# Optimization experiments

Hardware: AMD Instinct MI355X
Metric: run time of the kernel (lower is better)

Reference implementation:

```python
import jax, jax.numpy as jnp
import numpy as np

N, D, S, E, EL, ITERS = 250_000, 128, 6, 500_000, 50_000, 4


def setup_inputs() -> dict:
    key = jax.random.key(0)
    ks = jax.random.split(key, 16)
    s = 1.0 / np.sqrt(D)  # keep activations O(1)
    return {
        'feat':   jax.random.normal(ks[0], (N, D), jnp.float32),
        'pre_u':  jax.random.randint(ks[1], (S, E), 0, N, jnp.int32),
        'pre_v':  jax.random.randint(ks[2], (S, E), 0, N, jnp.int32),
        'suc_u':  jax.random.randint(ks[3], (S, E), 0, N, jnp.int32),
        'suc_v':  jax.random.randint(ks[4], (S, E), 0, N, jnp.int32),
        'left_u': jax.random.randint(ks[5], (EL,), 0, N, jnp.int32),
        'left_v': jax.random.randint(ks[6], (EL,), 0, N, jnp.int32),
        'right_u': jax.random.randint(ks[7], (EL,), 0, N, jnp.int32),
        'right_v': jax.random.randint(ks[8], (EL,), 0, N, jnp.int32),
        'W_ctr':   jax.random.normal(ks[9],  (ITERS, D, D), jnp.float32) * s,
        'W_pre':   jax.random.normal(ks[10], (ITERS, S, D, D), jnp.float32) * s,
        'W_suc':   jax.random.normal(ks[11], (ITERS, S, D, D), jnp.float32) * s,
        'W_left':  jax.random.normal(ks[12], (ITERS, D, D), jnp.float32) * s,
        'W_right': jax.random.normal(ks[13], (ITERS, D, D), jnp.float32) * s,
        'gn1_w': jnp.ones((ITERS, D), jnp.float32),
        'gn1_b': jnp.zeros((ITERS, D), jnp.float32),
        'W_ctr2':  jax.random.normal(ks[14], (ITERS, D, D), jnp.float32) * s,
        'gn2_w': jnp.ones((ITERS, D), jnp.float32),
        'gn2_b': jnp.zeros((ITERS, D), jnp.float32),
    }


def _gn(x, w, b, eps=1e-5):
    # torch GroupNorm(1, D) on a [N, D] input: per-row normalization over channels
    mu = jnp.mean(x, -1, keepdims=True)
    var = jnp.mean((x - mu) ** 2, -1, keepdims=True)
    return (x - mu) * jax.lax.rsqrt(var + eps) * w + b


def reference(feat, pre_u, pre_v, suc_u, suc_v, left_u, left_v, right_u, right_v,
              W_ctr, W_pre, W_suc, W_left, W_right, gn1_w, gn1_b,
              W_ctr2, gn2_w, gn2_b):
    res = feat
    for i in range(ITERS):  # 4 fusion iterations, structurally distinct weights
        temp = feat @ W_ctr[i].T  # nn.Linear(bias=False): x @ W.T
        for k in range(S):  # 6 dilation scales, pre and suc edges
            temp = temp.at[pre_u[k]].add(feat[pre_v[k]] @ W_pre[i, k].T)
            temp = temp.at[suc_u[k]].add(feat[suc_v[k]] @ W_suc[i, k].T)
        temp = temp.at[left_u].add(feat[left_v] @ W_left[i].T)
        temp = temp.at[right_u].add(feat[right_v] @ W_right[i].T)
        h = jax.nn.relu(_gn(temp, gn1_w[i], gn1_b[i]))           # fuse['norm'] + relu
        h = _gn(h @ W_ctr2[i].T, gn2_w[i], gn2_b[i])             # fuse['ctr2']: Linear+GN, no act
        feat = jax.nn.relu(h + res)                              # residual + relu
        res = feat
    return feat
```

## Files before the change

kernel.cpp:

```cpp
#include <hip/hip_runtime.h>


#define NN 250000
#define DD 128
#define EE 500000
#define ELE 50000
#define NITER 4
#define NL 14
#define M14 (NL*NN)
#define TOTE (12*EE + 2*ELE)
#define KBIG (15*DD)
#define BK 64
#define TILES_TOTAL ((NN + 127)/128)
#define NBKT TILES_TOTAL
#define BCAP 4096
#define LK (128*NL)
#define NBLK_BUCKET 256
#define EPB ((TOTE + NBLK_BUCKET - 1)/NBLK_BUCKET)

typedef unsigned short u16;
typedef __attribute__((ext_vector_type(4))) float f32x4;
typedef __attribute__((ext_vector_type(8))) __bf16 bf16x8;

static __device__ __forceinline__ unsigned f2bf(float f) {
  unsigned u = __float_as_uint(f);
  return (u + 0x7fffu + ((u >> 16) & 1u)) >> 16;
}
static __device__ __forceinline__ float bflo(unsigned w){ return __uint_as_float(w << 16); }
static __device__ __forceinline__ float bfhi(unsigned w){ return __uint_as_float(w & 0xffff0000u); }

static __device__ __forceinline__ void gload16(const u16* g, u16* l) {
  __builtin_amdgcn_global_load_lds(
      (const __attribute__((address_space(1))) void*)g,
      (__attribute__((address_space(3))) void*)l, 16, 0, 0);
}

static __device__ __forceinline__ int edge_u(int idx,
    const int* __restrict__ pu, const int* __restrict__ su,
    const int* __restrict__ lu, const int* __restrict__ ru) {
  if (idx < 12*EE) {
    int l = idx / EE; int e = idx - l*EE;
    return (l < 6) ? pu[l*EE + e] : su[(l-6)*EE + e];
  }
  int r = idx - 12*EE;
  return (r < ELE) ? lu[r] : ru[r - ELE];
}

static __device__ __forceinline__ void edge_luv(int idx,
    const int* __restrict__ pu, const int* __restrict__ pv,
    const int* __restrict__ su, const int* __restrict__ sv,
    const int* __restrict__ lu, const int* __restrict__ lv,
    const int* __restrict__ ru, const int* __restrict__ rv,
    int& l, int& u, int& v) {
  if (idx < 12*EE) {
    l = idx / EE; int e = idx - l*EE;
    if (l < 6) { u = pu[l*EE+e]; v = pv[l*EE+e]; }
    else       { u = su[(l-6)*EE+e]; v = sv[(l-6)*EE+e]; }
  } else {
    int r = idx - 12*EE;
    if (r < ELE) { l = 12; u = lu[r]; v = lv[r]; }
    else         { l = 13; u = ru[r-ELE]; v = rv[r-ELE]; }
  }
}

__global__ __launch_bounds__(1024) void k_bucket(
    const int* __restrict__ pu, const int* __restrict__ pv,
    const int* __restrict__ su, const int* __restrict__ sv,
    const int* __restrict__ lu, const int* __restrict__ lv,
    const int* __restrict__ ru, const int* __restrict__ rv,
    int* __restrict__ bcur, unsigned* __restrict__ bstage) {
  __shared__ int cnt[NBKT];
  __shared__ int cur[NBKT];
  int t = threadIdx.x;
  for (int i=t; i<NBKT; i+=1024) cnt[i] = 0;
  __syncthreads();
  int e0 = blockIdx.x * EPB;
  int e1 = e0 + EPB; if (e1 > TOTE) e1 = TOTE;
  for (int idx = e0 + t; idx < e1; idx += 1024) {
    int u = edge_u(idx, pu, su, lu, ru);
    atomicAdd(&cnt[u >> 7], 1);
  }
  __syncthreads();
  for (int i=t; i<NBKT; i+=1024) {
    int c = cnt[i];
    cur[i] = c ? atomicAdd(&bcur[i], c) : 0;
  }
  __syncthreads();
  for (int idx = e0 + t; idx < e1; idx += 1024) {
    int l, u, v;
    edge_luv(idx, pu, pv, su, sv, lu, lv, ru, rv, l, u, v);
    int b = u >> 7;
    unsigned rec = ((unsigned)((u & 127)*NL + l) << 18) | (unsigned)v;
    int pos = atomicAdd(&cur[b], 1);
    if (pos < BCAP) bstage[(size_t)b*BCAP + pos] = rec;
  }
}

__global__ void k_bscan(const int* __restrict__ bcur, int* __restrict__ bbase,
                        int* __restrict__ rowptr) {
  __shared__ int wsum[4];
  int t = threadIdx.x, lane = t & 63, w = t >> 6;
  int v[8]; int s = 0;
  #pragma unroll
  for (int j=0;j<8;j++){
    int idx = t*8 + j;
    int x = 0;
    if (idx < NBKT) { x = bcur[idx]; if (x > BCAP) x = BCAP; }
    v[j] = s; s += x;
  }
  int ps = s;
  for (int d=1; d<64; d<<=1) { int o = __shfl_up(ps, d); if (lane >= d) ps += o; }
  if (lane == 63) wsum[w] = ps;
  __syncthreads();
  int woff = 0;
  for (int j=0;j<w;j++) woff += wsum[j];
  int excl = woff + ps - s;
  #pragma unroll
  for (int j=0;j<8;j++){
    int idx = t*8 + j;
    if (idx < NBKT) bbase[idx] = excl + v[j];
  }
  if (t == 255) rowptr[M14] = excl + s;
}

__global__ __launch_bounds__(256) void k_place(const unsigned* __restrict__ bstage,
    const int* __restrict__ bcur, const int* __restrict__ bbase,
    int* __restrict__ rowptr, int* __restrict__ edge_v) {
  __shared__ int lh[LK];
  __shared__ int lex[LK];
  __shared__ int wsum[4];
  int b = blockIdx.x, t = threadIdx.x;
  int lane = t & 63, w = t >> 6;
  int cnt = bcur[b]; if (cnt > BCAP) cnt = BCAP;
  int base = bbase[b];
  const unsigned* rec = bstage + (size_t)b*BCAP;
  for (int i=t; i<LK; i+=256) lh[i] = 0;
  __syncthreads();
  for (int e=t; e<cnt; e+=256) atomicAdd(&lh[rec[e]>>18], 1);
  __syncthreads();
  int s = 0;
  int my[7];
  #pragma unroll
  for (int j=0;j<7;j++){ my[j] = s; s += lh[t*7+j]; }
  int ps = s;
  for (int d=1; d<64; d<<=1) { int o = __shfl_up(ps, d); if (lane >= d) ps += o; }
  if (lane == 63) wsum[w] = ps;
  __syncthreads();
  int woff = 0;
  for (int j=0;j<w;j++) woff += wsum[j];
  int excl = woff + ps - s;
  #pragma unroll
  for (int j=0;j<7;j++) lex[t*7+j] = excl + my[j];
  __syncthreads();
  for (int i=t; i<LK; i+=256) rowptr[(size_t)b*LK + i] = base + lex[i];
  for (int i=t; i<LK; i+=256) lh[i] = lex[i];
  __syncthreads();
  for (int e=t; e<cnt; e+=256) {
    unsigned r = rec[e];
    int pos = atomicAdd(&lh[r>>18], 1);
    edge_v[base + pos] = (int)(r & 0x3FFFFu);
  }
}

__global__ void k_f2bf(const float* __restrict__ in, unsigned* __restrict__ out) {
  int i = blockIdx.x*256 + threadIdx.x;
  float2 v = ((const float2*)in)[i];
  out[i] = f2bf(v.x) | (f2bf(v.y) << 16);
}

__global__ void k_bw(const float* __restrict__ Wc, const float* __restrict__ Wp,
                     const float* __restrict__ Ws, const float* __restrict__ Wl,
                     const float* __restrict__ Wr, const float* __restrict__ Wc2,
                     int it, u16* __restrict__ wcat, u16* __restrict__ wc2) {
  int i = blockIdx.x*256 + threadIdx.x;
  if (i < 128*KBIG) {
    int r = i / KBIG, K = i - r*KBIG;
    int s = K >> 7, c = K & 127;
    float val;
    if (s == 0)       val = Wc[(it*128 + r)*128 + c];
    else if (s <= 6)  val = Wp[((it*6 + (s-1))*128 + r)*128 + c];
    else if (s <= 12) val = Ws[((it*6 + (s-7))*128 + r)*128 + c];
    else if (s == 13) val = Wl[(it*128 + r)*128 + c];
    else              val = Wr[(it*128 + r)*128 + c];
    wcat[i] = (u16)f2bf(val);
  } else {
    int j = i - 128*KBIG;
    wc2[j] = (u16)f2bf(Wc2[it*16384 + j]);
  }
}

__global__ __launch_bounds__(256) void k_agg(const unsigned* __restrict__ featbf,
    const int* __restrict__ rowptr, const int* __restrict__ edge_v,
    unsigned* __restrict__ X, int chunk_base) {
  int wid = threadIdx.x >> 6, lane = threadIdx.x & 63;
  int nl = blockIdx.x*4 + wid;
  int node = chunk_base + nl;
  size_t xb = (size_t)nl * (14*64);
  if (node >= NN) {
    #pragma unroll
    for (int s=0;s<14;s++) X[xb + s*64 + lane] = 0;
    return;
  }
  int rp = 0;
  if (lane < 15) rp = rowptr[node*NL + lane];
  int st0 = __shfl(rp, 0);
  int cnt = __shfl(rp, 14) - st0;
  float ax = 0.f, ay = 0.f;
  int s = 0;
  int nextb = __shfl(rp, 1);
  int vv = 0;
  for (int base = 0; base < cnt; base += 8) {
    if ((base & 63) == 0) vv = edge_v[st0 + base + lane];
    unsigned wrow[8];
    int m = cnt - base; if (m > 8) m = 8;
    #pragma unroll
    for (int q=0;q<8;q++)
      if (q < m) {
        int v = __shfl(vv, (base & 63) + q);
        wrow[q] = featbf[(size_t)v*64 + lane];
      }
    for (int q=0;q<m;q++) {
      int e = st0 + base + q;
      while (e == nextb && s < 14) {
        X[xb + s*64 + lane] = f2bf(ax) | (f2bf(ay) << 16);
        ax = 0.f; ay = 0.f; s++;
        int ni = s + 1; if (ni > 14) ni = 14;
        nextb = __shfl(rp, ni);
      }
      ax += bflo(wrow[q]); ay += bfhi(wrow[q]);
    }
  }
  while (s < 14) {
    X[xb + s*64 + lane] = f2bf(ax) | (f2bf(ay) << 16);
    ax = 0.f; ay = 0.f; s++;
  }
}

__global__ __launch_bounds__(256) void gemm_fused(
    const u16* __restrict__ Xc, const u16* __restrict__ fbf,
    const u16* __restrict__ Bw, const u16* __restrict__ wc2g,
    unsigned* __restrict__ fout, float* __restrict__ out32, int last,
    const float* __restrict__ g1w, const float* __restrict__ g1b,
    const float* __restrict__ g2w, const float* __restrict__ g2b,
    int row0_abs) {
  __shared__ u16 smem[2*128*BK];
  __shared__ float stats[2][128][2];
  u16* As = smem; u16* Bs = smem + 128*BK;
  int tid = threadIdx.x, wid = tid >> 6, lane = tid & 63;
  int wm = wid >> 1, wn = wid & 1;
  int g = lane >> 4, l15 = lane & 15, l7 = lane & 7;
  int tile_row = blockIdx.x * 128;
  f32x4 acc[4][4] = {};
  int srow8 = lane >> 3;
  int scol = ((lane & 7) ^ srow8) * 8;
  for (int k0 = 0; k0 < KBIG; k0 += BK) {
    __syncthreads();
    if (k0 < DD) {
      #pragma unroll
      for (int j=0;j<4;j++) {
        int seg = wid + j*4; int r = seg*8 + srow8;
        int arow = row0_abs + tile_row + r; if (arow > NN-1) arow = NN-1;
        gload16(fbf + (size_t)arow*DD + (k0 + scol), &As[seg*512]);
        gload16(Bw + (size_t)r*KBIG + (k0 + scol), &Bs[seg*512]);
      }
    } else {
      #pragma unroll
      for (int j=0;j<4;j++) {
        int seg = wid + j*4; int r = seg*8 + srow8;
        gload16(Xc + (size_t)(tile_row + r)*(14*128) + (k0 - DD + scol), &As[seg*512]);
        gload16(Bw + (size_t)r*KBIG + (k0 + scol), &Bs[seg*512]);
      }
    }
    __syncthreads();
    #pragma unroll
    for (int kk=0; kk<2; kk++) {
      bf16x8 af[4], bfr[4];
      #pragma unroll
      for (int mt=0; mt<4; mt++)
        af[mt] = *(const bf16x8*)&As[((wm*64 + mt*16 + l15)*BK + kk*32 + g*8) ^ (l7<<3)];
      #pragma unroll
      for (int nt=0; nt<4; nt++)
        bfr[nt] = *(const bf16x8*)&Bs[((wn*64 + nt*16 + l15)*BK + kk*32 + g*8) ^ (l7<<3)];
      #pragma unroll
      for (int mt=0; mt<4; mt++)
        #pragma unroll
        for (int nt=0; nt<4; nt++)
          acc[mt][nt] = __builtin_amdgcn_mfma_f32_16x16x32_bf16(af[mt], bfr[nt], acc[mt][nt], 0, 0, 0);
    }
  }
  __syncthreads();

  #pragma unroll
  for (int mt=0; mt<4; mt++)
    #pragma unroll
    for (int r=0; r<4; r++) {
      float s = 0.f, q = 0.f;
      #pragma unroll
      for (int nt=0; nt<4; nt++) { float v = acc[mt][nt][r]; s += v; q += v*v; }
      #pragma unroll
      for (int d=1; d<16; d<<=1) { s += __shfl_xor(s, d); q += __shfl_xor(q, d); }
      if (l15 == 0) {
        int R = wm*64 + mt*16 + g*4 + r;
        stats[wn][R][0] = s; stats[wn][R][1] = q;
      }
    }
  __syncthreads();

  float w1[4], b1[4], w2[4], b2[4];
  #pragma unroll
  for (int nt=0; nt<4; nt++) {
    int C = wn*64 + nt*16 + l15;
    w1[nt] = g1w[C]; b1[nt] = g1b[C];
    w2[nt] = g2w[C]; b2[nt] = g2b[C];
  }
  #pragma unroll
  for (int mt=0; mt<4; mt++)
    #pragma unroll
    for (int r=0; r<4; r++) {
      int R = wm*64 + mt*16 + g*4 + r;
      float ts = stats[0][R][0] + stats[1][R][0];
      float tq = stats[0][R][1] + stats[1][R][1];
      float mu = ts*(1.f/DD), var = tq*(1.f/DD) - mu*mu;
      float rs = rsqrtf(var + 1e-5f);
      #pragma unroll
      for (int nt=0; nt<4; nt++) {
        int C = wn*64 + nt*16 + l15;
        float y = fmaxf(fmaf((acc[mt][nt][r]-mu)*rs, w1[nt], b1[nt]), 0.f);
        float p = __shfl_xor(y, 1);
        if (!(lane & 1)) {
          unsigned word = f2bf(y) | (f2bf(p) << 16);
          int idx = (R*128 + (C & ~1)) ^ ((R&7)<<3);
          *(unsigned*)&smem[idx] = word;
        }
      }
    }
  __syncthreads();

  f32x4 a2[4][4] = {};
  #pragma unroll
  for (int kk2=0; kk2<4; kk2++) {
    bf16x8 wf[4], hf[4];
    #pragma unroll
    for (int nt=0; nt<4; nt++)
      wf[nt] = *(const bf16x8*)&wc2g[(size_t)(wn*64 + nt*16 + l15)*DD + kk2*32 + g*8];
    #pragma unroll
    for (int mt=0; mt<4; mt++)
      hf[mt] = *(const bf16x8*)&smem[((wm*64 + mt*16 + l15)*DD + kk2*32 + g*8) ^ (l7<<3)];
    #pragma unroll
    for (int mt=0; mt<4; mt++)
      #pragma unroll
      for (int nt=0; nt<4; nt++)
        a2[mt][nt] = __builtin_amdgcn_mfma_f32_16x16x32_bf16(hf[mt], wf[nt], a2[mt][nt], 0, 0, 0);
  }
  __syncthreads();

  #pragma unroll
  for (int mt=0; mt<4; mt++)
    #pragma unroll
    for (int r=0; r<4; r++) {
      float s = 0.f, q = 0.f;
      #pragma unroll
      for (int nt=0; nt<4; nt++) { float v = a2[mt][nt][r]; s += v; q += v*v; }
      #pragma unroll
      for (int d=1; d<16; d<<=1) { s += __shfl_xor(s, d); q += __shfl_xor(q, d); }
      if (l15 == 0) {
        int R = wm*64 + mt*16 + g*4 + r;
        stats[wn][R][0] = s; stats[wn][R][1] = q;
      }
    }
  __syncthreads();

  #pragma unroll
  for (int mt=0; mt<4; mt++)
    #pragma unroll
    for (int r=0; r<4; r++) {
      int R = wm*64 + mt*16 + g*4 + r;
      int grow = row0_abs + tile_row + R;
      float ts = stats[0][R][0] + stats[1][R][0];
      float tq = stats[0][R][1] + stats[1][R][1];
      float mu = ts*(1.f/DD), var = tq*(1.f/DD) - mu*mu;
      float rs = rsqrtf(var + 1e-5f);
      bool ok = grow < NN;
      #pragma unroll
      for (int nt=0; nt<4; nt++) {
        int C = wn*64 + nt*16 + l15;
        float yv = fmaf((a2[mt][nt][r]-mu)*rs, w2[nt], b2[nt]);
        unsigned rw = ok ? ((const unsigned*)fbf)[(size_t)grow*64 + (C>>1)] : 0u;
        float resv = (lane & 1) ? bfhi(rw) : bflo(rw);
        float o = fmaxf(yv + resv, 0.f);
        if (last && ok) out32[(size_t)grow*DD + C] = o;
        float p = __shfl_xor(o, 1);
        if (!(lane & 1) && ok)
          fout[(size_t)grow*64 + (C>>1)] = f2bf(o) | (f2bf(p) << 16);
      }
    }
}

extern "C" void kernel_launch(void* const* d_in, const int* in_sizes, int n_in,
                              void* d_out, int out_size, void* d_ws, size_t ws_size,
                              hipStream_t stream) {
  const float* feat_in = (const float*)d_in[0];
  const int* pre_u  = (const int*)d_in[1];
  const int* pre_v  = (const int*)d_in[2];
  const int* suc_u  = (const int*)d_in[3];
  const int* suc_v  = (const int*)d_in[4];
  const int* left_u = (const int*)d_in[5];
  const int* left_v = (const int*)d_in[6];
  const int* right_u= (const int*)d_in[7];
  const int* right_v= (const int*)d_in[8];
  const float* W_ctr  = (const float*)d_in[9];
  const float* W_pre  = (const float*)d_in[10];
  const float* W_suc  = (const float*)d_in[11];
  const float* W_left = (const float*)d_in[12];
  const float* W_right= (const float*)d_in[13];
  const float* gn1w   = (const float*)d_in[14];
  const float* gn1b   = (const float*)d_in[15];
  const float* W_ctr2 = (const float*)d_in[16];
  const float* gn2w   = (const float*)d_in[17];
  const float* gn2b   = (const float*)d_in[18];

  char* ws = (char*)d_ws;
  size_t off = 0;
  auto alloc = [&](size_t bytes) -> char* {
    char* p = ws + off; off += (bytes + 255) & ~(size_t)255; return p;
  };
  unsigned* featA  = (unsigned*)alloc((size_t)NN*64*4);
  unsigned* featB  = (unsigned*)alloc((size_t)NN*64*4);
  u16*      wcat   = (u16*)     alloc((size_t)128*KBIG*2);
  u16*      wc2    = (u16*)     alloc((size_t)128*128*2);
  int*      rowptr = (int*)     alloc(((size_t)NBKT*LK + 1)*4);
  int*      edge_v = (int*)     alloc((size_t)(TOTE + 64)*4);
  unsigned* bstage = (unsigned*)alloc((size_t)NBKT*BCAP*4);
  int*      bcur   = (int*)     alloc((size_t)NBKT*4);
  int*      bbase  = (int*)     alloc((size_t)NBKT*4);

  size_t tile_bytes = (size_t)128*(14*128)*2;
  size_t avail = (ws_size > off + 65536) ? (ws_size - off - 65536) : 0;
  int chunk_tiles = (int)(avail / tile_bytes);
  if (chunk_tiles > 256) chunk_tiles = 256;
  if (chunk_tiles < 8) chunk_tiles = 8;
  unsigned* Xc = (unsigned*)alloc((size_t)chunk_tiles * tile_bytes);
  int nchunk = (TILES_TOTAL + chunk_tiles - 1) / chunk_tiles;
  (void)in_sizes; (void)n_in; (void)out_size;

  hipMemsetAsync(bcur, 0, (size_t)NBKT*4, stream);
  k_bucket<<<NBLK_BUCKET, 1024, 0, stream>>>(pre_u, pre_v, suc_u, suc_v,
                                             left_u, left_v, right_u, right_v,
                                             bcur, bstage);
  k_bscan<<<1, 256, 0, stream>>>(bcur, bbase, rowptr);
  k_place<<<NBKT, 256, 0, stream>>>(bstage, bcur, bbase, rowptr, edge_v);

  k_f2bf<<<NN*64/256, 256, 0, stream>>>(feat_in, featA);

  for (int it = 0; it < NITER; it++) {
    unsigned* fin  = (it & 1) ? featB : featA;
    unsigned* fo   = (it & 1) ? featA : featB;
    int last = (it == NITER-1) ? 1 : 0;
    k_bw<<<1024, 256, 0, stream>>>(W_ctr, W_pre, W_suc, W_left, W_right, W_ctr2, it, wcat, wc2);
    for (int c = 0; c < nchunk; c++) {
      int tile0 = c*chunk_tiles;
      int tiles = (TILES_TOTAL - tile0 < chunk_tiles) ? (TILES_TOTAL - tile0) : chunk_tiles;
      int base  = tile0*128;
      k_agg<<<tiles*32, 256, 0, stream>>>(fin, rowptr, edge_v, Xc, base);
      gemm_fused<<<tiles, 256, 0, stream>>>((const u16*)Xc, (const u16*)fin, wcat, wc2,
                                            fo, (float*)d_out, last,
                                            gn1w + it*DD, gn1b + it*DD,
                                            gn2w + it*DD, gn2b + it*DD, base);
    }
  }
}
```

Measured before the change: 4.765 ms.

## Fuse edge aggregation into GEMM tile, gathering into LDS double buffer

Removes the separate k_agg kernel and the chunked global Xc intermediate. The CSR is now sorted per tile by (slot, local row), so each warp in gemm_fused gathers and sums neighbor rows for 32 rows of the next slot straight into a swizzled LDS buffer while MFMAs run on the current buffer. This drops the round trip of the 14-slot aggregated activations through global memory and most kernel launches. In exchange, weights are read directly from global memory with no LDS staging, aggregation runs with only 4 warps per tile (about 1954 blocks), and load balance inside a block now depends on per-slot edge counts.

```diff
diff --git a/kernel.cpp b/kernel.cpp
--- a/kernel.cpp
+++ b/kernel.cpp
@@ -10,7 +10,6 @@
 #define M14 (NL*NN)
 #define TOTE (12*EE + 2*ELE)
 #define KBIG (15*DD)
-#define BK 64
 #define TILES_TOTAL ((NN + 127)/128)
 #define NBKT TILES_TOTAL
 #define BCAP 4096
@@ -90,7 +89,7 @@
     int l, u, v;
     edge_luv(idx, pu, pv, su, sv, lu, lv, ru, rv, l, u, v);
     int b = u >> 7;
-    unsigned rec = ((unsigned)((u & 127)*NL + l) << 18) | (unsigned)v;
+    unsigned rec = ((unsigned)((l << 7) | (u & 127)) << 18) | (unsigned)v;
     int pos = atomicAdd(&cur[b], 1);
     if (pos < BCAP) bstage[(size_t)b*BCAP + pos] = rec;
   }
@@ -125,7 +124,7 @@
 
 __global__ __launch_bounds__(256) void k_place(const unsigned* __restrict__ bstage,
     const int* __restrict__ bcur, const int* __restrict__ bbase,
-    int* __restrict__ rowptr, int* __restrict__ edge_v) {
+    int* __restrict__ rowptr, unsigned* __restrict__ edge_v) {
   __shared__ int lh[LK];
   __shared__ int lex[LK];
   __shared__ int wsum[4];
@@ -157,8 +156,9 @@
   __syncthreads();
   for (int e=t; e<cnt; e+=256) {
     unsigned r = rec[e];
-    int pos = atomicAdd(&lh[r>>18], 1);
-    edge_v[base + pos] = (int)(r & 0x3FFFFu);
+    unsigned key = r >> 18;
+    int pos = atomicAdd(&lh[key], 1);
+    edge_v[base + pos] = ((key & 127u) << 18) | (r & 0x3FFFFu);
   }
 }
 
@@ -189,106 +189,90 @@
   }
 }
 
-__global__ __launch_bounds__(256) void k_agg(const unsigned* __restrict__ featbf,
-    const int* __restrict__ rowptr, const int* __restrict__ edge_v,
-    unsigned* __restrict__ X, int chunk_base) {
-  int wid = threadIdx.x >> 6, lane = threadIdx.x & 63;
-  int nl = blockIdx.x*4 + wid;
-  int node = chunk_base + nl;
-  size_t xb = (size_t)nl * (14*64);
-  if (node >= NN) {
-    #pragma unroll
-    for (int s=0;s<14;s++) X[xb + s*64 + lane] = 0;
-    return;
-  }
-  int rp = 0;
-  if (lane < 15) rp = rowptr[node*NL + lane];
-  int st0 = __shfl(rp, 0);
-  int cnt = __shfl(rp, 14) - st0;
-  float ax = 0.f, ay = 0.f;
-  int s = 0;
-  int nextb = __shfl(rp, 1);
-  int vv = 0;
-  for (int base = 0; base < cnt; base += 8) {
-    if ((base & 63) == 0) vv = edge_v[st0 + base + lane];
-    unsigned wrow[8];
-    int m = cnt - base; if (m > 8) m = 8;
-    #pragma unroll
-    for (int q=0;q<8;q++)
-      if (q < m) {
-        int v = __shfl(vv, (base & 63) + q);
-        wrow[q] = featbf[(size_t)v*64 + lane];
-      }
-    for (int q=0;q<m;q++) {
-      int e = st0 + base + q;
-      while (e == nextb && s < 14) {
-        X[xb + s*64 + lane] = f2bf(ax) | (f2bf(ay) << 16);
-        ax = 0.f; ay = 0.f; s++;
-        int ni = s + 1; if (ni > 14) ni = 14;
-        nextb = __shfl(rp, ni);
-      }
-      ax += bflo(wrow[q]); ay += bfhi(wrow[q]);
-    }
-  }
-  while (s < 14) {
-    X[xb + s*64 + lane] = f2bf(ax) | (f2bf(ay) << 16);
-    ax = 0.f; ay = 0.f; s++;
-  }
-}
-
 __global__ __launch_bounds__(256) void gemm_fused(
-    const u16* __restrict__ Xc, const u16* __restrict__ fbf,
-    const u16* __restrict__ Bw, const u16* __restrict__ wc2g,
+    const unsigned* __restrict__ fbf, const u16* __restrict__ Bw,
+    const u16* __restrict__ wc2g,
+    const int* __restrict__ rowptr, const unsigned* __restrict__ edge_v,
     unsigned* __restrict__ fout, float* __restrict__ out32, int last,
     const float* __restrict__ g1w, const float* __restrict__ g1b,
-    const float* __restrict__ g2w, const float* __restrict__ g2b,
-    int row0_abs) {
-  __shared__ u16 smem[2*128*BK];
-  __shared__ float stats[2][128][2];
-  u16* As = smem; u16* Bs = smem + 128*BK;
+    const float* __restrict__ g2w, const float* __restrict__ g2b) {
+  __shared__ u16 smem[2*128*128];
   int tid = threadIdx.x, wid = tid >> 6, lane = tid & 63;
   int wm = wid >> 1, wn = wid & 1;
   int g = lane >> 4, l15 = lane & 15, l7 = lane & 7;
-  int tile_row = blockIdx.x * 128;
+  int t = blockIdx.x;
+  int tile_row = t * 128;
   f32x4 acc[4][4] = {};
-  int srow8 = lane >> 3;
-  int scol = ((lane & 7) ^ srow8) * 8;
-  for (int k0 = 0; k0 < KBIG; k0 += BK) {
+
+  #pragma unroll
+  for (int j=0;j<8;j++) {
+    int rb = j*16 + wid*4;
+    int r = rb + (lane>>4);
+    int arow = tile_row + r; if (arow > NN-1) arow = NN-1;
+    gload16((const u16*)fbf + (size_t)arow*128 + (((lane&15) ^ (r&7))<<3),
+            smem + rb*128);
+  }
+
+  for (int s = 0; s < 15; ++s) {
+    if (s < 14) {
+      u16* dst = smem + (((s+1)&1) << 14);
+      int base_r = wid*32;
+      size_t rpb = (size_t)t*LK + s*128 + base_r;
+      int st0 = rowptr[rpb];
+      int en  = rowptr[rpb + 32];
+      float ax = 0.f, ay = 0.f;
+      int cur = base_r;
+      unsigned recs = 0;
+      for (int eb = st0; eb < en; eb += 8) {
+        int off = (eb - st0) & 63;
+        if (off == 0) { int e = eb + lane; recs = (e < en) ? edge_v[e] : 0; }
+        int m = en - eb; if (m > 8) m = 8;
+        unsigned wrow[8]; int rr[8];
+        #pragma unroll
+        for (int q=0;q<8;q++) if (q < m) {
+          unsigned rq = __shfl(recs, off + q);
+          rr[q] = (int)(rq >> 18);
+          wrow[q] = fbf[(size_t)(rq & 0x3FFFFu)*64 + lane];
+        }
+        #pragma unroll 1
+        for (int q=0;q<m;q++) {
+          int r = rr[q];
+          while (cur < r) {
+            *(unsigned*)&dst[(cur*128 + 2*lane) ^ ((cur&7)<<3)] =
+                f2bf(ax) | (f2bf(ay) << 16);
+            ax = 0.f; ay = 0.f; cur++;
+          }
+          ax += bflo(wrow[q]); ay += bfhi(wrow[q]);
+        }
+      }
+      while (cur < base_r + 32) {
+        *(unsigned*)&dst[(cur*128 + 2*lane) ^ ((cur&7)<<3)] =
+            f2bf(ax) | (f2bf(ay) << 16);
+        ax = 0.f; ay = 0.f; cur++;
+      }
+    }
     __syncthreads();
-    if (k0 < DD) {
-      #pragma unroll
-      for (int j=0;j<4;j++) {
-        int seg = wid + j*4; int r = seg*8 + srow8;
-        int arow = row0_abs + tile_row + r; if (arow > NN-1) arow = NN-1;
-        gload16(fbf + (size_t)arow*DD + (k0 + scol), &As[seg*512]);
-        gload16(Bw + (size_t)r*KBIG + (k0 + scol), &Bs[seg*512]);
-      }
-    } else {
-      #pragma unroll
-      for (int j=0;j<4;j++) {
-        int seg = wid + j*4; int r = seg*8 + srow8;
-        gload16(Xc + (size_t)(tile_row + r)*(14*128) + (k0 - DD + scol), &As[seg*512]);
-        gload16(Bw + (size_t)r*KBIG + (k0 + scol), &Bs[seg*512]);
-      }
-    }
-    __syncthreads();
-    #pragma unroll
-    for (int kk=0; kk<2; kk++) {
-      bf16x8 af[4], bfr[4];
+    const u16* abuf = smem + ((s&1) << 14);
+    #pragma unroll
+    for (int kk=0; kk<4; kk++) {
+      bf16x8 af[4], wf[4];
+      #pragma unroll
+      for (int nt=0; nt<4; nt++)
+        wf[nt] = *(const bf16x8*)&Bw[(size_t)(wn*64 + nt*16 + l15)*KBIG + s*128 + kk*32 + g*8];
       #pragma unroll
       for (int mt=0; mt<4; mt++)
-        af[mt] = *(const bf16x8*)&As[((wm*64 + mt*16 + l15)*BK + kk*32 + g*8) ^ (l7<<3)];
-      #pragma unroll
-      for (int nt=0; nt<4; nt++)
-        bfr[nt] = *(const bf16x8*)&Bs[((wn*64 + nt*16 + l15)*BK + kk*32 + g*8) ^ (l7<<3)];
+        af[mt] = *(const bf16x8*)&abuf[((wm*64 + mt*16 + l15)*128 + kk*32 + g*8) ^ (l7<<3)];
       #pragma unroll
       for (int mt=0; mt<4; mt++)
         #pragma unroll
         for (int nt=0; nt<4; nt++)
-          acc[mt][nt] = __builtin_amdgcn_mfma_f32_16x16x32_bf16(af[mt], bfr[nt], acc[mt][nt], 0, 0, 0);
-    }
-  }
-  __syncthreads();
+          acc[mt][nt] = __builtin_amdgcn_mfma_f32_16x16x32_bf16(af[mt], wf[nt], acc[mt][nt], 0, 0, 0);
+    }
+    __syncthreads();
+  }
+
+  float* stats = (float*)smem;
+  u16* hbuf = smem + 16384;
 
   #pragma unroll
   for (int mt=0; mt<4; mt++)
@@ -301,7 +285,7 @@
       for (int d=1; d<16; d<<=1) { s += __shfl_xor(s, d); q += __shfl_xor(q, d); }
       if (l15 == 0) {
         int R = wm*64 + mt*16 + g*4 + r;
-        stats[wn][R][0] = s; stats[wn][R][1] = q;
+        stats[(wn*128 + R)*2 + 0] = s; stats[(wn*128 + R)*2 + 1] = q;
       }
     }
   __syncthreads();
@@ -318,8 +302,8 @@
     #pragma unroll
     for (int r=0; r<4; r++) {
       int R = wm*64 + mt*16 + g*4 + r;
-      float ts = stats[0][R][0] + stats[1][R][0];
-      float tq = stats[0][R][1] + stats[1][R][1];
+      float ts = stats[R*2] + stats[(128+R)*2];
+      float tq = stats[R*2+1] + stats[(128+R)*2+1];
       float mu = ts*(1.f/DD), var = tq*(1.f/DD) - mu*mu;
       float rs = rsqrtf(var + 1e-5f);
       #pragma unroll
@@ -329,8 +313,7 @@
         float p = __shfl_xor(y, 1);
         if (!(lane & 1)) {
           unsigned word = f2bf(y) | (f2bf(p) << 16);
-          int idx = (R*128 + (C & ~1)) ^ ((R&7)<<3);
-          *(unsigned*)&smem[idx] = word;
+          *(unsigned*)&hbuf[(R*128 + (C & ~1)) ^ ((R&7)<<3)] = word;
         }
       }
     }
@@ -345,7 +328,7 @@
       wf[nt] = *(const bf16x8*)&wc2g[(size_t)(wn*64 + nt*16 + l15)*DD + kk2*32 + g*8];
     #pragma unroll
     for (int mt=0; mt<4; mt++)
-      hf[mt] = *(const bf16x8*)&smem[((wm*64 + mt*16 + l15)*DD + kk2*32 + g*8) ^ (l7<<3)];
+      hf[mt] = *(const bf16x8*)&hbuf[((wm*64 + mt*16 + l15)*128 + kk2*32 + g*8) ^ (l7<<3)];
     #pragma unroll
     for (int mt=0; mt<4; mt++)
       #pragma unroll
@@ -365,7 +348,7 @@
       for (int d=1; d<16; d<<=1) { s += __shfl_xor(s, d); q += __shfl_xor(q, d); }
       if (l15 == 0) {
         int R = wm*64 + mt*16 + g*4 + r;
-        stats[wn][R][0] = s; stats[wn][R][1] = q;
+        stats[(wn*128 + R)*2 + 0] = s; stats[(wn*128 + R)*2 + 1] = q;
       }
     }
   __syncthreads();
@@ -375,9 +358,9 @@
     #pragma unroll
     for (int r=0; r<4; r++) {
       int R = wm*64 + mt*16 + g*4 + r;
-      int grow = row0_abs + tile_row + R;
-      float ts = stats[0][R][0] + stats[1][R][0];
-      float tq = stats[0][R][1] + stats[1][R][1];
+      int grow = tile_row + R;
+      float ts = stats[R*2] + stats[(128+R)*2];
+      float tq = stats[R*2+1] + stats[(128+R)*2+1];
       float mu = ts*(1.f/DD), var = tq*(1.f/DD) - mu*mu;
       float rs = rsqrtf(var + 1e-5f);
       bool ok = grow < NN;
@@ -385,7 +368,7 @@
       for (int nt=0; nt<4; nt++) {
         int C = wn*64 + nt*16 + l15;
         float yv = fmaf((a2[mt][nt][r]-mu)*rs, w2[nt], b2[nt]);
-        unsigned rw = ok ? ((const unsigned*)fbf)[(size_t)grow*64 + (C>>1)] : 0u;
+        unsigned rw = ok ? fbf[(size_t)grow*64 + (C>>1)] : 0u;
         float resv = (lane & 1) ? bfhi(rw) : bflo(rw);
         float o = fmaxf(yv + resv, 0.f);
         if (last && ok) out32[(size_t)grow*DD + C] = o;
@@ -429,19 +412,11 @@
   u16*      wcat   = (u16*)     alloc((size_t)128*KBIG*2);
   u16*      wc2    = (u16*)     alloc((size_t)128*128*2);
   int*      rowptr = (int*)     alloc(((size_t)NBKT*LK + 1)*4);
-  int*      edge_v = (int*)     alloc((size_t)(TOTE + 64)*4);
+  unsigned* edge_v = (unsigned*)alloc((size_t)(TOTE + 64)*4);
   unsigned* bstage = (unsigned*)alloc((size_t)NBKT*BCAP*4);
   int*      bcur   = (int*)     alloc((size_t)NBKT*4);
   int*      bbase  = (int*)     alloc((size_t)NBKT*4);
-
-  size_t tile_bytes = (size_t)128*(14*128)*2;
-  size_t avail = (ws_size > off + 65536) ? (ws_size - off - 65536) : 0;
-  int chunk_tiles = (int)(avail / tile_bytes);
-  if (chunk_tiles > 256) chunk_tiles = 256;
-  if (chunk_tiles < 8) chunk_tiles = 8;
-  unsigned* Xc = (unsigned*)alloc((size_t)chunk_tiles * tile_bytes);
-  int nchunk = (TILES_TOTAL + chunk_tiles - 1) / chunk_tiles;
-  (void)in_sizes; (void)n_in; (void)out_size;
+  (void)in_sizes; (void)n_in; (void)out_size; (void)ws_size;
 
   hipMemsetAsync(bcur, 0, (size_t)NBKT*4, stream);
   k_bucket<<<NBLK_BUCKET, 1024, 0, stream>>>(pre_u, pre_v, suc_u, suc_v,
@@ -453,19 +428,13 @@
   k_f2bf<<<NN*64/256, 256, 0, stream>>>(feat_in, featA);
 
   for (int it = 0; it < NITER; it++) {
-    unsigned* fin  = (it & 1) ? featB : featA;
-    unsigned* fo   = (it & 1) ? featA : featB;
+    unsigned* fin = (it & 1) ? featB : featA;
+    unsigned* fo  = (it & 1) ? featA : featB;
     int last = (it == NITER-1) ? 1 : 0;
     k_bw<<<1024, 256, 0, stream>>>(W_ctr, W_pre, W_suc, W_left, W_right, W_ctr2, it, wcat, wc2);
-    for (int c = 0; c < nchunk; c++) {
-      int tile0 = c*chunk_tiles;
-      int tiles = (TILES_TOTAL - tile0 < chunk_tiles) ? (TILES_TOTAL - tile0) : chunk_tiles;
-      int base  = tile0*128;
-      k_agg<<<tiles*32, 256, 0, stream>>>(fin, rowptr, edge_v, Xc, base);
-      gemm_fused<<<tiles, 256, 0, stream>>>((const u16*)Xc, (const u16*)fin, wcat, wc2,
-                                            fo, (float*)d_out, last,
-                                            gn1w + it*DD, gn1b + it*DD,
-                                            gn2w + it*DD, gn2b + it*DD, base);
-    }
-  }
-}
+    gemm_fused<<<TILES_TOTAL, 256, 0, stream>>>(fin, wcat, wc2, rowptr, edge_v,
+                                                fo, (float*)d_out, last,
+                                                gn1w + it*DD, gn1b + it*DD,
+                                                gn2w + it*DD, gn2b + it*DD);
+  }
+}
```

Result: slower. 8.802 ms (+84.7%).
